# Optimization experiments

Measured on AMD Instinct MI355X. Metric: run time of the kernel, lower is better.

Reference implementation:

```python
import math
import jax
import jax.numpy as jnp
import numpy as np
from jax import lax

B, L, D_MODEL, N_HEADS, C = 4, 2048, 512, 8, 1
D_HEAD = D_MODEL // N_HEADS


def setup_inputs() -> dict:
    key = jax.random.key(0)
    ks = jax.random.split(key, 7)
    s = 0.02  # stand-in for glorot init scale
    return {
        "queries": jax.random.normal(ks[0], (B, L, D_MODEL), jnp.float32),
        "keys": jax.random.normal(ks[1], (B, L, D_MODEL), jnp.float32),
        "values": jax.random.normal(ks[2], (B, L, D_MODEL), jnp.float32),
        "wq": jax.random.normal(ks[3], (D_MODEL, D_MODEL), jnp.float32) * s,
        "wk": jax.random.normal(ks[4], (D_MODEL, D_MODEL), jnp.float32) * s,
        "wv": jax.random.normal(ks[5], (D_MODEL, D_MODEL), jnp.float32) * s,
        "wo": jax.random.normal(ks[6], (D_MODEL, D_MODEL), jnp.float32) * s,
    }


def reference(queries, keys, values, wq, wk, wv, wo):
    b, len_q, _ = queries.shape
    len_k = keys.shape[1]
    # QKV projections, split into heads: [B, H, L, Dh]
    Q = (queries @ wq).reshape(b, len_q, N_HEADS, D_HEAD).transpose(0, 2, 1, 3)
    K = (keys @ wk).reshape(b, len_k, N_HEADS, D_HEAD).transpose(0, 2, 1, 3)
    V = (values @ wv).reshape(b, len_k, N_HEADS, D_HEAD).transpose(0, 2, 1, 3)
    # full O(L^2) correlation as in the original, then mean over heads & query idx
    corr = jnp.einsum("bhid,bhjd->bhij", Q, K)  # [B, H, Lq, Lk]
    mean_corr = corr.mean(axis=(1, 2))  # [B, Lk]
    # top-k delay selection (k = max(1, int(c * log(Lq))), static at trace time)
    k = max(1, int(C * math.log(max(2, len_q))))
    topk_vals, topk_idx = lax.top_k(mean_corr, k)  # [B, k]
    weights = jax.nn.softmax(topk_vals, axis=-1)  # [B, k]
    # vectorized circular roll: rolled[b,i,h,t,d] = V[b,h,(t+delay_bi) % L, d]
    idx = (jnp.arange(len_k)[None, None, :] + topk_idx[:, :, None]) % len_k  # [B,k,L]
    gathered = jnp.take_along_axis(
        V[:, None],  # [B, 1, H, L, Dh]
        idx[:, :, None, :, None],  # [B, k, 1, L, 1]
        axis=3,
    )  # [B, k, H, L, Dh]
    agg = jnp.einsum("bk,bkhld->bhld", weights.astype(V.dtype), gathered)
    out = agg.transpose(0, 2, 1, 3).reshape(b, len_q, D_MODEL) @ wo
    return out
```

## Files before the change

kernel.cpp:

```cpp
#include <hip/hip_runtime.h>
#include <hip/hip_bf16.h>

#define DMODEL 512
#define LEN 2048
#define NBATCH 4
#define TOPK 7
#define LDK 40

typedef __attribute__((ext_vector_type(8))) short short8;
typedef __attribute__((ext_vector_type(4))) float floatx4;

__device__ __forceinline__ float b2f(ushort h) {
  union { uint u; float f; } c; c.u = ((uint)h) << 16; return c.f;
}
__device__ __forceinline__ ushort f2b(float f) {
  union { float f; uint u; } c; c.f = f;
  uint u = c.u;
  uint r = (u + 0x7fffu + ((u >> 16) & 1u)) >> 16;
  return (ushort)r;
}

__device__ __forceinline__ float ld1(const void* p, size_t i, int bf) {
  return bf ? b2f(((const ushort*)p)[i]) : ((const float*)p)[i];
}
__device__ __forceinline__ void ld4v(const void* p, size_t i, int bf, float* o) {
  if (bf) {
    uint2 v = *(const uint2*)((const ushort*)p + i);
    const ushort* s = (const ushort*)&v;
#pragma unroll
    for (int j = 0; j < 4; ++j) o[j] = b2f(s[j]);
  } else {
    float4 a = *(const float4*)((const float*)p + i);
    o[0] = a.x; o[1] = a.y; o[2] = a.z; o[3] = a.w;
  }
}
__device__ __forceinline__ void ld8v(const void* p, size_t i, int bf, float* o) {
  if (bf) {
    uint4 v = *(const uint4*)((const ushort*)p + i);
    const ushort* s = (const ushort*)&v;
#pragma unroll
    for (int j = 0; j < 8; ++j) o[j] = b2f(s[j]);
  } else {
    float4 a = *(const float4*)((const float*)p + i);
    float4 b = *(const float4*)((const float*)p + i + 4);
    o[0] = a.x; o[1] = a.y; o[2] = a.z; o[3] = a.w;
    o[4] = b.x; o[5] = b.y; o[6] = b.z; o[7] = b.w;
  }
}

__global__ void detect_dtype(const uint* __restrict__ probe, int* __restrict__ flag) {
  __shared__ int cnt[512];
  int t = threadIdx.x;
  uint u = probe[t];
  uint e = (u >> 7) & 0xFFu;
  cnt[t] = (e < 90u || e > 140u) ? 1 : 0;
  __syncthreads();
  for (int s = 256; s > 0; s >>= 1) {
    if (t < s) cnt[t] += cnt[t + s];
    __syncthreads();
  }
  if (t == 0) *flag = (cnt[0] < 50) ? 1 : 0;
}

__global__ void qsum_part(const void* __restrict__ q, float* __restrict__ P,
                          const int* __restrict__ flag) {
  int bf = *flag;
  int b = blockIdx.x >> 5, c = blockIdx.x & 31;
  int d = threadIdx.x;
  size_t base = (((size_t)b * LEN + (size_t)c * 64) << 9) + d;
  float acc = 0.f;
#pragma unroll 8
  for (int l = 0; l < 64; ++l) acc += ld1(q, base + ((size_t)l << 9), bf);
  P[(size_t)blockIdx.x * DMODEL + d] = acc;
}

__global__ void qbar_k(const float* __restrict__ P, const void* __restrict__ wq,
                       float* __restrict__ qb, const int* __restrict__ flag) {
  __shared__ float qs[DMODEL];
  __shared__ float red[4][64];
  int bf = *flag;
  int b = blockIdx.x >> 3, g = blockIdx.x & 7;
  int t = threadIdx.x;
  for (int d = t; d < DMODEL; d += 256) {
    float a = 0.f;
#pragma unroll
    for (int c = 0; c < 32; ++c) a += P[(size_t)(b * 32 + c) * DMODEL + d];
    qs[d] = a;
  }
  __syncthreads();
  int part = t >> 6, jl = t & 63;
  int j = g * 64 + jl;
  float acc = 0.f;
  int d0 = part * 128;
#pragma unroll 8
  for (int d = d0; d < d0 + 128; ++d)
    acc += qs[d] * ld1(wq, (size_t)d * DMODEL + j, bf);
  red[part][jl] = acc;
  __syncthreads();
  if (part == 0)
    qb[(size_t)b * DMODEL + j] = red[0][jl] + red[1][jl] + red[2][jl] + red[3][jl];
}

__global__ void u_k(const float* __restrict__ qb, const void* __restrict__ wk,
                    float* __restrict__ u, const int* __restrict__ flag) {
  int bf = *flag;
  int gw = (blockIdx.x * 256 + threadIdx.x) >> 6;
  int lane = threadIdx.x & 63;
  int b = gw >> 9, t = gw & 511;
  float kv[8];
  ld8v(wk, (size_t)t * DMODEL + lane * 8, bf, kv);
  const float* qbb = qb + (size_t)b * DMODEL + lane * 8;
  float acc = 0.f;
#pragma unroll
  for (int i = 0; i < 8; ++i) acc += kv[i] * qbb[i];
#pragma unroll
  for (int off = 32; off > 0; off >>= 1) acc += __shfl_down(acc, off);
  if (lane == 0) u[(size_t)b * DMODEL + t] = acc;
}

__global__ void mean_corr_k(const void* __restrict__ keys,
                            const float* __restrict__ u,
                            float* __restrict__ mc,
                            const int* __restrict__ flag) {
  int bf = *flag;
  int wid = (blockIdx.x * 256 + threadIdx.x) >> 6;
  int lane = threadIdx.x & 63;
  int b = wid >> 11, j = wid & (LEN - 1);
  float kv[8];
  ld8v(keys, (((size_t)b * LEN + j) << 9) + lane * 8, bf, kv);
  const float* ub = u + (size_t)b * DMODEL + lane * 8;
  float acc = 0.f;
#pragma unroll
  for (int i = 0; i < 8; ++i) acc += kv[i] * ub[i];
#pragma unroll
  for (int off = 32; off > 0; off >>= 1) acc += __shfl_down(acc, off);
  if (lane == 0) mc[(size_t)b * LEN + j] = acc * (1.f / 16384.f);
}

__global__ void topk_softmax(const float* __restrict__ mc,
                             float* __restrict__ wts, int* __restrict__ dls) {
  __shared__ float vals[LEN];
  __shared__ float rv[4];
  __shared__ int ri[4];
  __shared__ float bv_s[TOPK];
  __shared__ int bi_s[TOPK];
  int b = blockIdx.x, t = threadIdx.x;
  for (int i = t; i < LEN; i += 256) vals[i] = mc[(size_t)b * LEN + i];
  __syncthreads();
  for (int it = 0; it < TOPK; ++it) {
    float bv = -3.0e38f; int bi = 0;
#pragma unroll
    for (int c = 0; c < LEN / 256; ++c) {
      int i = t + c * 256;
      float v = vals[i];
      if (v > bv) { bv = v; bi = i; }
    }
#pragma unroll
    for (int off = 32; off > 0; off >>= 1) {
      float ov = __shfl_down(bv, off);
      int   oi = __shfl_down(bi, off);
      if (ov > bv || (ov == bv && oi < bi)) { bv = ov; bi = oi; }
    }
    if ((t & 63) == 0) { rv[t >> 6] = bv; ri[t >> 6] = bi; }
    __syncthreads();
    if (t == 0) {
      float fv = rv[0]; int fi = ri[0];
      for (int w = 1; w < 4; ++w)
        if (rv[w] > fv || (rv[w] == fv && ri[w] < fi)) { fv = rv[w]; fi = ri[w]; }
      bv_s[it] = fv; bi_s[it] = fi;
      vals[fi] = -3.0e38f;
    }
    __syncthreads();
  }
  if (t == 0) {
    float m = bv_s[0];
    float e[TOPK], s = 0.f;
#pragma unroll
    for (int i = 0; i < TOPK; ++i) { e[i] = __expf(bv_s[i] - m); s += e[i]; }
    float inv = 1.f / s;
#pragma unroll
    for (int i = 0; i < TOPK; ++i) {
      wts[b * 8 + i] = e[i] * inv;
      dls[b * 8 + i] = bi_s[i];
    }
  }
}

__global__ __launch_bounds__(256) void gemm_w2(
    const void* __restrict__ A, const void* __restrict__ B,
    ushort* __restrict__ W2T, const int* __restrict__ flag) {
  __shared__ ushort As[64 * LDK];
  __shared__ ushort Bs[64 * LDK];
  __shared__ ushort Ts[64 * 72];
  int bf = *flag;
  int t = threadIdx.x;
  int n0 = blockIdx.x * 64, m0 = blockIdx.y * 64;
  int w = t >> 6, lane = t & 63;
  int quad = lane >> 4, l16 = lane & 15;
  floatx4 acc[4] = {{0,0,0,0},{0,0,0,0},{0,0,0,0},{0,0,0,0}};
  int am = t >> 2, ak = (t & 3) * 8;
  int kp = t >> 4, nb = (t & 15) * 4;

  for (int k0 = 0; k0 < DMODEL; k0 += 32) {
    float a8[8];
    ld8v(A, (size_t)(m0 + am) * DMODEL + k0 + ak, bf, a8);
    union { ushort s[8]; uint4 v; } ap;
#pragma unroll
    for (int j = 0; j < 8; ++j) ap.s[j] = f2b(a8[j]);
    *(uint4*)(&As[am * LDK + ak]) = ap.v;

    float b0[4], b1[4];
    ld4v(B, (size_t)(k0 + 2 * kp) * DMODEL + n0 + nb, bf, b0);
    ld4v(B, (size_t)(k0 + 2 * kp + 1) * DMODEL + n0 + nb, bf, b1);
#pragma unroll
    for (int i = 0; i < 4; ++i) {
      ushort2 pr; pr.x = f2b(b0[i]); pr.y = f2b(b1[i]);
      *(ushort2*)(&Bs[(nb + i) * LDK + 2 * kp]) = pr;
    }
    __syncthreads();

    short8 af = *(const short8*)(&As[(w * 16 + l16) * LDK + quad * 8]);
#pragma unroll
    for (int c = 0; c < 4; ++c) {
      short8 bfr = *(const short8*)(&Bs[(c * 16 + l16) * LDK + quad * 8]);
      acc[c] = __builtin_amdgcn_mfma_f32_16x16x32_bf16(af, bfr, acc[c], 0, 0, 0);
    }
    __syncthreads();
  }
#pragma unroll
  for (int c = 0; c < 4; ++c) {
    int cl = c * 16 + l16;
#pragma unroll
    for (int r = 0; r < 4; ++r)
      Ts[cl * 72 + (w * 16 + quad * 4 + r)] = f2b(acc[c][r]);
  }
  __syncthreads();
  int nl = t >> 2, ch = t & 3;
  uint4 v0 = *(const uint4*)(&Ts[nl * 72 + ch * 16]);
  uint4 v1 = *(const uint4*)(&Ts[nl * 72 + ch * 16 + 8]);
  ushort* dst = W2T + (size_t)(n0 + nl) * DMODEL + m0 + ch * 16;
  *(uint4*)dst = v0;
  *(uint4*)(dst + 8) = v1;
}

__global__ void mix_k(const void* __restrict__ values,
                      const float* __restrict__ wts, const int* __restrict__ dls,
                      ushort* __restrict__ Amix, const int* __restrict__ flag) {
  int bf = *flag;
  int t = threadIdx.x;
  int row = blockIdx.x * 4 + (t >> 6);
  int lane = t & 63;
  int b = row >> 11, l = row & (LEN - 1);
  float w[TOPK]; int dl[TOPK];
#pragma unroll
  for (int i = 0; i < TOPK; ++i) { w[i] = wts[b * 8 + i]; dl[i] = dls[b * 8 + i]; }
  float acc[8] = {0,0,0,0,0,0,0,0};
#pragma unroll
  for (int i = 0; i < TOPK; ++i) {
    int src = (l + dl[i]) & (LEN - 1);
    float v[8];
    ld8v(values, (((size_t)b * LEN + src) << 9) + lane * 8, bf, v);
#pragma unroll
    for (int j = 0; j < 8; ++j) acc[j] += w[i] * v[j];
  }
  union { ushort o[8]; uint4 v; } pk;
#pragma unroll
  for (int j = 0; j < 8; ++j) pk.o[j] = f2b(acc[j]);
  *(uint4*)(Amix + ((size_t)row << 9) + lane * 8) = pk.v;
}

__global__ __launch_bounds__(256) void gemm_out(
    const ushort* __restrict__ Amix, const ushort* __restrict__ W2T,
    void* __restrict__ out, const int* __restrict__ flag) {
  __shared__ ushort As[128 * LDK];
  __shared__ ushort Bs[128 * LDK];
  int bf = *flag;
  int t = threadIdx.x;
  int n0 = blockIdx.x * 128, m0 = blockIdx.y * 128;
  int w = t >> 6, lane = t & 63;
  int quad = lane >> 4, l16 = lane & 15;
  int wr = (w & 1) * 64, wc = (w >> 1) * 64;
  floatx4 acc[4][4];
#pragma unroll
  for (int r = 0; r < 4; ++r)
#pragma unroll
    for (int c = 0; c < 4; ++c) acc[r][c] = (floatx4){0, 0, 0, 0};
  int sr = t >> 2, sc = (t & 3) * 8;

  for (int k0 = 0; k0 < DMODEL; k0 += 32) {
    *(uint4*)(&As[sr * LDK + sc])        = *(const uint4*)(Amix + (size_t)(m0 + sr) * DMODEL + k0 + sc);
    *(uint4*)(&As[(sr + 64) * LDK + sc]) = *(const uint4*)(Amix + (size_t)(m0 + sr + 64) * DMODEL + k0 + sc);
    *(uint4*)(&Bs[sr * LDK + sc])        = *(const uint4*)(W2T + (size_t)(n0 + sr) * DMODEL + k0 + sc);
    *(uint4*)(&Bs[(sr + 64) * LDK + sc]) = *(const uint4*)(W2T + (size_t)(n0 + sr + 64) * DMODEL + k0 + sc);
    __syncthreads();
    short8 af[4], bfg[4];
#pragma unroll
    for (int r = 0; r < 4; ++r)
      af[r] = *(const short8*)(&As[(wr + r * 16 + l16) * LDK + quad * 8]);
#pragma unroll
    for (int c = 0; c < 4; ++c)
      bfg[c] = *(const short8*)(&Bs[(wc + c * 16 + l16) * LDK + quad * 8]);
#pragma unroll
    for (int r = 0; r < 4; ++r)
#pragma unroll
      for (int c = 0; c < 4; ++c)
        acc[r][c] = __builtin_amdgcn_mfma_f32_16x16x32_bf16(af[r], bfg[c], acc[r][c], 0, 0, 0);
    __syncthreads();
  }
#pragma unroll
  for (int r = 0; r < 4; ++r) {
    int row = m0 + wr + r * 16 + quad * 4;
#pragma unroll
    for (int c = 0; c < 4; ++c) {
      int col = n0 + wc + c * 16 + l16;
#pragma unroll
      for (int rr = 0; rr < 4; ++rr) {
        size_t oidx = (size_t)(row + rr) * DMODEL + col;
        float v = acc[r][c][rr];
        if (bf) ((ushort*)out)[oidx] = f2b(v);
        else    ((float*)out)[oidx] = v;
      }
    }
  }
}

extern "C" void kernel_launch(void* const* d_in, const int* in_sizes, int n_in,
                              void* d_out, int out_size, void* d_ws, size_t ws_size,
                              hipStream_t stream) {
  const void* queries = d_in[0];
  const void* keys    = d_in[1];
  const void* values  = d_in[2];
  const void* wq      = d_in[3];
  const void* wk      = d_in[4];
  const void* wv      = d_in[5];
  const void* wo      = d_in[6];

  char* ws = (char*)d_ws;
  float* P     = (float*)(ws + 0);
  ushort* W2T  = (ushort*)(ws + 262144);
  float* QB    = (float*)(ws + 786432);
  float* U     = (float*)(ws + 794624);
  float* MC    = (float*)(ws + 802816);
  float* WT    = (float*)(ws + 835584);
  int*   DL    = (int*)  (ws + 835712);
  int*   FLAG  = (int*)  (ws + 835840);
  ushort* AMIX = (ushort*)(ws + 1048576);

  detect_dtype<<<1, 512, 0, stream>>>((const uint*)wq, FLAG);
  gemm_w2<<<dim3(8, 8), 256, 0, stream>>>(wv, wo, W2T, FLAG);
  qsum_part<<<NBATCH * 32, 512, 0, stream>>>(queries, P, FLAG);
  qbar_k<<<NBATCH * 8, 256, 0, stream>>>(P, wq, QB, FLAG);
  u_k<<<NBATCH * 512 / 4, 256, 0, stream>>>(QB, wk, U, FLAG);
  mean_corr_k<<<NBATCH * LEN / 4, 256, 0, stream>>>(keys, U, MC, FLAG);
  topk_softmax<<<NBATCH, 256, 0, stream>>>(MC, WT, DL);
  mix_k<<<NBATCH * LEN / 4, 256, 0, stream>>>(values, WT, DL, AMIX, FLAG);
  gemm_out<<<dim3(4, 64), 256, 0, stream>>>(AMIX, W2T, d_out, FLAG);
}
```

Before: 177.9 us.

## Fuse dtype detection, query sum, W2 GEMM and value bf16 conversion into one prep kernel

Drops the separate dtype-detect kernel; every kernel now re-detects the dtype inline with a one-wave reduction over the weight probe. Merges the query partial sums, the Wv@Wo GEMM and a new pass that converts values to a bf16 copy into a single launch, cutting the launch count. mix_k then gathers the 7 shifted rows from the half-size bf16 copy instead of the fp32 values. The cost is an extra full write and read of the values tensor in bf16, plus some redundant probe reads in each block.

```diff
diff --git a/kernel.cpp b/kernel.cpp
--- a/kernel.cpp
+++ b/kernel.cpp
@@ -48,43 +48,120 @@
   }
 }
 
-__global__ void detect_dtype(const uint* __restrict__ probe, int* __restrict__ flag) {
-  __shared__ int cnt[512];
-  int t = threadIdx.x;
-  uint u = probe[t];
-  uint e = (u >> 7) & 0xFFu;
-  cnt[t] = (e < 90u || e > 140u) ? 1 : 0;
+__device__ __forceinline__ int detect_bf16(const void* probe) {
+  __shared__ int s_flag;
+  int t = threadIdx.x;
+  if (t < 64) {
+    const uint4* p = (const uint4*)probe;
+    uint4 a = p[t * 2];
+    uint4 b = p[t * 2 + 1];
+    uint w[8] = {a.x, a.y, a.z, a.w, b.x, b.y, b.z, b.w};
+    int c = 0;
+#pragma unroll
+    for (int j = 0; j < 8; ++j) {
+      uint e = (w[j] >> 7) & 0xFFu;
+      c += (e < 90u || e > 140u) ? 1 : 0;
+    }
+#pragma unroll
+    for (int off = 32; off > 0; off >>= 1) c += __shfl_down(c, off);
+    if (t == 0) s_flag = (c < 50) ? 1 : 0;
+  }
   __syncthreads();
-  for (int s = 256; s > 0; s >>= 1) {
-    if (t < s) cnt[t] += cnt[t + s];
-    __syncthreads();
-  }
-  if (t == 0) *flag = (cnt[0] < 50) ? 1 : 0;
-}
-
-__global__ void qsum_part(const void* __restrict__ q, float* __restrict__ P,
-                          const int* __restrict__ flag) {
-  int bf = *flag;
-  int b = blockIdx.x >> 5, c = blockIdx.x & 31;
-  int d = threadIdx.x;
-  size_t base = (((size_t)b * LEN + (size_t)c * 64) << 9) + d;
-  float acc = 0.f;
+  return s_flag;
+}
+
+__global__ __launch_bounds__(256) void prep_k(
+    const void* __restrict__ queries, const void* __restrict__ values,
+    const void* __restrict__ wv, const void* __restrict__ wo,
+    const void* __restrict__ probe,
+    float* __restrict__ P, ushort* __restrict__ VB, ushort* __restrict__ W2T) {
+  __shared__ ushort As[64 * LDK];
+  __shared__ ushort Bs[64 * LDK];
+  __shared__ ushort Ts[64 * 72];
+  int bf = detect_bf16(probe);
+  int blk = blockIdx.x;
+  int t = threadIdx.x;
+  if (blk < 256) {
+    int b = blk >> 6, c = blk & 63;
+    size_t base = (((size_t)b * LEN + (size_t)c * 32) << 9) + t;
+    float a0 = 0.f, a1 = 0.f;
 #pragma unroll 8
-  for (int l = 0; l < 64; ++l) acc += ld1(q, base + ((size_t)l << 9), bf);
-  P[(size_t)blockIdx.x * DMODEL + d] = acc;
-}
-
-__global__ void qbar_k(const float* __restrict__ P, const void* __restrict__ wq,
-                       float* __restrict__ qb, const int* __restrict__ flag) {
+    for (int l = 0; l < 32; ++l) {
+      a0 += ld1(queries, base + ((size_t)l << 9), bf);
+      a1 += ld1(queries, base + ((size_t)l << 9) + 256, bf);
+    }
+    P[(size_t)blk * DMODEL + t] = a0;
+    P[(size_t)blk * DMODEL + t + 256] = a1;
+  } else if (blk < 2304) {
+    int r = (blk - 256) * 4 + (t >> 6);
+    int lane = t & 63;
+    float v[8];
+    ld8v(values, ((size_t)r << 9) + lane * 8, bf, v);
+    union { ushort o[8]; uint4 u; } pk;
+#pragma unroll
+    for (int j = 0; j < 8; ++j) pk.o[j] = f2b(v[j]);
+    *(uint4*)(VB + ((size_t)r << 9) + lane * 8) = pk.u;
+  } else {
+    int wb = blk - 2304;
+    int n0 = (wb & 7) * 64, m0 = (wb >> 3) * 64;
+    int w = t >> 6, lane = t & 63;
+    int quad = lane >> 4, l16 = lane & 15;
+    floatx4 acc[4] = {{0,0,0,0},{0,0,0,0},{0,0,0,0},{0,0,0,0}};
+    int am = t >> 2, ak = (t & 3) * 8;
+    int kp = t >> 4, nb = (t & 15) * 4;
+    for (int k0 = 0; k0 < DMODEL; k0 += 32) {
+      float a8[8];
+      ld8v(wv, (size_t)(m0 + am) * DMODEL + k0 + ak, bf, a8);
+      union { ushort s[8]; uint4 v; } ap;
+#pragma unroll
+      for (int j = 0; j < 8; ++j) ap.s[j] = f2b(a8[j]);
+      *(uint4*)(&As[am * LDK + ak]) = ap.v;
+      float b0[4], b1[4];
+      ld4v(wo, (size_t)(k0 + 2 * kp) * DMODEL + n0 + nb, bf, b0);
+      ld4v(wo, (size_t)(k0 + 2 * kp + 1) * DMODEL + n0 + nb, bf, b1);
+#pragma unroll
+      for (int i = 0; i < 4; ++i) {
+        ushort2 pr; pr.x = f2b(b0[i]); pr.y = f2b(b1[i]);
+        *(ushort2*)(&Bs[(nb + i) * LDK + 2 * kp]) = pr;
+      }
+      __syncthreads();
+      short8 af = *(const short8*)(&As[(w * 16 + l16) * LDK + quad * 8]);
+#pragma unroll
+      for (int c = 0; c < 4; ++c) {
+        short8 bfr = *(const short8*)(&Bs[(c * 16 + l16) * LDK + quad * 8]);
+        acc[c] = __builtin_amdgcn_mfma_f32_16x16x32_bf16(af, bfr, acc[c], 0, 0, 0);
+      }
+      __syncthreads();
+    }
+#pragma unroll
+    for (int c = 0; c < 4; ++c) {
+      int cl = c * 16 + l16;
+#pragma unroll
+      for (int r = 0; r < 4; ++r)
+        Ts[cl * 72 + (w * 16 + quad * 4 + r)] = f2b(acc[c][r]);
+    }
+    __syncthreads();
+    int nl = t >> 2, ch = t & 3;
+    uint4 v0 = *(const uint4*)(&Ts[nl * 72 + ch * 16]);
+    uint4 v1 = *(const uint4*)(&Ts[nl * 72 + ch * 16 + 8]);
+    ushort* dst = W2T + (size_t)(n0 + nl) * DMODEL + m0 + ch * 16;
+    *(uint4*)dst = v0;
+    *(uint4*)(dst + 8) = v1;
+  }
+}
+
+__global__ __launch_bounds__(256) void qbar_k(
+    const float* __restrict__ P, const void* __restrict__ wq,
+    float* __restrict__ qb) {
   __shared__ float qs[DMODEL];
   __shared__ float red[4][64];
-  int bf = *flag;
+  int bf = detect_bf16(wq);
   int b = blockIdx.x >> 3, g = blockIdx.x & 7;
   int t = threadIdx.x;
   for (int d = t; d < DMODEL; d += 256) {
     float a = 0.f;
 #pragma unroll
-    for (int c = 0; c < 32; ++c) a += P[(size_t)(b * 32 + c) * DMODEL + d];
+    for (int c = 0; c < 64; ++c) a += P[(size_t)(b * 64 + c) * DMODEL + d];
     qs[d] = a;
   }
   __syncthreads();
@@ -101,9 +178,10 @@
     qb[(size_t)b * DMODEL + j] = red[0][jl] + red[1][jl] + red[2][jl] + red[3][jl];
 }
 
-__global__ void u_k(const float* __restrict__ qb, const void* __restrict__ wk,
-                    float* __restrict__ u, const int* __restrict__ flag) {
-  int bf = *flag;
+__global__ __launch_bounds__(256) void u_k(
+    const float* __restrict__ qb, const void* __restrict__ wk,
+    float* __restrict__ u, const void* __restrict__ probe) {
+  int bf = detect_bf16(probe);
   int gw = (blockIdx.x * 256 + threadIdx.x) >> 6;
   int lane = threadIdx.x & 63;
   int b = gw >> 9, t = gw & 511;
@@ -118,11 +196,10 @@
   if (lane == 0) u[(size_t)b * DMODEL + t] = acc;
 }
 
-__global__ void mean_corr_k(const void* __restrict__ keys,
-                            const float* __restrict__ u,
-                            float* __restrict__ mc,
-                            const int* __restrict__ flag) {
-  int bf = *flag;
+__global__ __launch_bounds__(256) void mean_corr_k(
+    const void* __restrict__ keys, const float* __restrict__ u,
+    float* __restrict__ mc, const void* __restrict__ probe) {
+  int bf = detect_bf16(probe);
   int wid = (blockIdx.x * 256 + threadIdx.x) >> 6;
   int lane = threadIdx.x & 63;
   int b = wid >> 11, j = wid & (LEN - 1);
@@ -186,67 +263,9 @@
   }
 }
 
-__global__ __launch_bounds__(256) void gemm_w2(
-    const void* __restrict__ A, const void* __restrict__ B,
-    ushort* __restrict__ W2T, const int* __restrict__ flag) {
-  __shared__ ushort As[64 * LDK];
-  __shared__ ushort Bs[64 * LDK];
-  __shared__ ushort Ts[64 * 72];
-  int bf = *flag;
-  int t = threadIdx.x;
-  int n0 = blockIdx.x * 64, m0 = blockIdx.y * 64;
-  int w = t >> 6, lane = t & 63;
-  int quad = lane >> 4, l16 = lane & 15;
-  floatx4 acc[4] = {{0,0,0,0},{0,0,0,0},{0,0,0,0},{0,0,0,0}};
-  int am = t >> 2, ak = (t & 3) * 8;
-  int kp = t >> 4, nb = (t & 15) * 4;
-
-  for (int k0 = 0; k0 < DMODEL; k0 += 32) {
-    float a8[8];
-    ld8v(A, (size_t)(m0 + am) * DMODEL + k0 + ak, bf, a8);
-    union { ushort s[8]; uint4 v; } ap;
-#pragma unroll
-    for (int j = 0; j < 8; ++j) ap.s[j] = f2b(a8[j]);
-    *(uint4*)(&As[am * LDK + ak]) = ap.v;
-
-    float b0[4], b1[4];
-    ld4v(B, (size_t)(k0 + 2 * kp) * DMODEL + n0 + nb, bf, b0);
-    ld4v(B, (size_t)(k0 + 2 * kp + 1) * DMODEL + n0 + nb, bf, b1);
-#pragma unroll
-    for (int i = 0; i < 4; ++i) {
-      ushort2 pr; pr.x = f2b(b0[i]); pr.y = f2b(b1[i]);
-      *(ushort2*)(&Bs[(nb + i) * LDK + 2 * kp]) = pr;
-    }
-    __syncthreads();
-
-    short8 af = *(const short8*)(&As[(w * 16 + l16) * LDK + quad * 8]);
-#pragma unroll
-    for (int c = 0; c < 4; ++c) {
-      short8 bfr = *(const short8*)(&Bs[(c * 16 + l16) * LDK + quad * 8]);
-      acc[c] = __builtin_amdgcn_mfma_f32_16x16x32_bf16(af, bfr, acc[c], 0, 0, 0);
-    }
-    __syncthreads();
-  }
-#pragma unroll
-  for (int c = 0; c < 4; ++c) {
-    int cl = c * 16 + l16;
-#pragma unroll
-    for (int r = 0; r < 4; ++r)
-      Ts[cl * 72 + (w * 16 + quad * 4 + r)] = f2b(acc[c][r]);
-  }
-  __syncthreads();
-  int nl = t >> 2, ch = t & 3;
-  uint4 v0 = *(const uint4*)(&Ts[nl * 72 + ch * 16]);
-  uint4 v1 = *(const uint4*)(&Ts[nl * 72 + ch * 16 + 8]);
-  ushort* dst = W2T + (size_t)(n0 + nl) * DMODEL + m0 + ch * 16;
-  *(uint4*)dst = v0;
-  *(uint4*)(dst + 8) = v1;
-}
-
-__global__ void mix_k(const void* __restrict__ values,
-                      const float* __restrict__ wts, const int* __restrict__ dls,
-                      ushort* __restrict__ Amix, const int* __restrict__ flag) {
-  int bf = *flag;
+__global__ __launch_bounds__(256) void mix_k(
+    const ushort* __restrict__ VB, const float* __restrict__ wts,
+    const int* __restrict__ dls, ushort* __restrict__ Amix) {
   int t = threadIdx.x;
   int row = blockIdx.x * 4 + (t >> 6);
   int lane = t & 63;
@@ -258,10 +277,10 @@
 #pragma unroll
   for (int i = 0; i < TOPK; ++i) {
     int src = (l + dl[i]) & (LEN - 1);
-    float v[8];
-    ld8v(values, (((size_t)b * LEN + src) << 9) + lane * 8, bf, v);
-#pragma unroll
-    for (int j = 0; j < 8; ++j) acc[j] += w[i] * v[j];
+    uint4 v = *(const uint4*)(VB + (((size_t)b * LEN + src) << 9) + lane * 8);
+    const ushort* vs = (const ushort*)&v;
+#pragma unroll
+    for (int j = 0; j < 8; ++j) acc[j] += w[i] * b2f(vs[j]);
   }
   union { ushort o[8]; uint4 v; } pk;
 #pragma unroll
@@ -271,10 +290,10 @@
 
 __global__ __launch_bounds__(256) void gemm_out(
     const ushort* __restrict__ Amix, const ushort* __restrict__ W2T,
-    void* __restrict__ out, const int* __restrict__ flag) {
+    void* __restrict__ out, const void* __restrict__ probe) {
   __shared__ ushort As[128 * LDK];
   __shared__ ushort Bs[128 * LDK];
-  int bf = *flag;
+  int bf = detect_bf16(probe);
   int t = threadIdx.x;
   int n0 = blockIdx.x * 128, m0 = blockIdx.y * 128;
   int w = t >> 6, lane = t & 63;
@@ -336,23 +355,21 @@
   const void* wo      = d_in[6];
 
   char* ws = (char*)d_ws;
-  float* P     = (float*)(ws + 0);
-  ushort* W2T  = (ushort*)(ws + 262144);
-  float* QB    = (float*)(ws + 786432);
-  float* U     = (float*)(ws + 794624);
-  float* MC    = (float*)(ws + 802816);
-  float* WT    = (float*)(ws + 835584);
-  int*   DL    = (int*)  (ws + 835712);
-  int*   FLAG  = (int*)  (ws + 835840);
-  ushort* AMIX = (ushort*)(ws + 1048576);
-
-  detect_dtype<<<1, 512, 0, stream>>>((const uint*)wq, FLAG);
-  gemm_w2<<<dim3(8, 8), 256, 0, stream>>>(wv, wo, W2T, FLAG);
-  qsum_part<<<NBATCH * 32, 512, 0, stream>>>(queries, P, FLAG);
-  qbar_k<<<NBATCH * 8, 256, 0, stream>>>(P, wq, QB, FLAG);
-  u_k<<<NBATCH * 512 / 4, 256, 0, stream>>>(QB, wk, U, FLAG);
-  mean_corr_k<<<NBATCH * LEN / 4, 256, 0, stream>>>(keys, U, MC, FLAG);
+  float*  P    = (float*)(ws + 0);
+  ushort* W2T  = (ushort*)(ws + 524288);
+  float*  QB   = (float*)(ws + 1048576);
+  float*  U    = (float*)(ws + 1056768);
+  float*  MC   = (float*)(ws + 1064960);
+  float*  WT   = (float*)(ws + 1097728);
+  int*    DL   = (int*)  (ws + 1097856);
+  ushort* VB   = (ushort*)(ws + 2097152);
+  ushort* AMIX = (ushort*)(ws + 10485760);
+
+  prep_k<<<2368, 256, 0, stream>>>(queries, values, wv, wo, wq, P, VB, W2T);
+  qbar_k<<<NBATCH * 8, 256, 0, stream>>>(P, wq, QB);
+  u_k<<<NBATCH * 512 / 4, 256, 0, stream>>>(QB, wk, U, wq);
+  mean_corr_k<<<NBATCH * LEN / 4, 256, 0, stream>>>(keys, U, MC, wq);
   topk_softmax<<<NBATCH, 256, 0, stream>>>(MC, WT, DL);
-  mix_k<<<NBATCH * LEN / 4, 256, 0, stream>>>(values, WT, DL, AMIX, FLAG);
-  gemm_out<<<dim3(4, 64), 256, 0, stream>>>(AMIX, W2T, d_out, FLAG);
-}
+  mix_k<<<NBATCH * LEN / 4, 256, 0, stream>>>(VB, WT, DL, AMIX);
+  gemm_out<<<dim3(4, 64), 256, 0, stream>>>(AMIX, W2T, d_out, wq);
+}
```

Result: faster. 167.1 us (-6.0%).
